# Kernel tuning notes

Measured on AMD Instinct MI355X. Metric: run time of the kernel, lower is better.

## Reference

```python
import jax, jax.numpy as jnp
import numpy as np

B, L, G, HID, H, D = 2, 4096, 256, 768, 12, 64
R = 127            # local_radius
BLK = R + 1        # block_len = 128
N = L // BLK       # 32 blocks (L divisible by BLK)
W = 2 * R + 1      # 255 local window
V = 32             # relative vocab size


def setup_inputs() -> dict:
    ks = jax.random.split(jax.random.key(0), 40)
    inp = {}
    inp["long_input"] = jax.random.normal(ks[0], (B, L, HID), jnp.float32)
    inp["global_input"] = jax.random.normal(ks[1], (B, G, HID), jnp.float32)
    inp["l2l_att_mask"] = jax.random.randint(ks[2], (B, L, W), 0, 2, jnp.int32)
    inp["g2g_att_mask"] = jax.random.randint(ks[3], (B, G, G), 0, 2, jnp.int32)
    inp["l2g_att_mask"] = jax.random.randint(ks[4], (B, L, G), 0, 2, jnp.int32)
    inp["g2l_att_mask"] = jax.random.randint(ks[5], (B, G, L), 0, 2, jnp.int32)
    inp["l2l_relative_att_ids"] = jax.random.randint(ks[6], (B, L, W), 0, V, jnp.int32)
    inp["g2g_relative_att_ids"] = jax.random.randint(ks[7], (B, G, G), 0, V, jnp.int32)
    inp["l2g_relative_att_ids"] = jax.random.randint(ks[8], (B, L, G), 0, V, jnp.int32)
    inp["g2l_relative_att_ids"] = jax.random.randint(ks[9], (B, G, L), 0, V, jnp.int32)
    i = 10
    for nm in ["q_long", "k_long", "v_long", "q_glob", "k_glob", "v_glob"]:
        inp["w" + nm] = 0.02 * jax.random.normal(ks[i], (HID, H * D), jnp.float32); i += 1
        inp["b" + nm] = jnp.zeros((H * D,), jnp.float32)
    inp["rel_emb_long"] = 0.5 * jax.random.normal(ks[i], (V, H, D), jnp.float32); i += 1
    inp["rel_bias_long"] = jnp.zeros((V, H), jnp.float32)
    inp["rel_emb_glob"] = 0.5 * jax.random.normal(ks[i], (V, H, D), jnp.float32); i += 1
    inp["rel_bias_glob"] = jnp.zeros((V, H), jnp.float32)
    inp["wo_long"] = 0.02 * jax.random.normal(ks[i], (H * D, HID), jnp.float32); i += 1
    inp["bo_long"] = jnp.zeros((HID,), jnp.float32)
    inp["wo_glob"] = 0.02 * jax.random.normal(ks[i], (H * D, HID), jnp.float32); i += 1
    inp["bo_glob"] = jnp.zeros((HID,), jnp.float32)
    return inp


def _expand_local(x):
    """[B, L, W] local-window ids -> blocked [B, N, BLK, 3*BLK] (skew + pad),
    zeroing entries outside the local window or outside the sequence."""
    xb = x.reshape(B, N, BLK, W)
    p = jnp.arange(BLK)[:, None]        # query pos within block
    c = jnp.arange(3 * BLK)[None, :]    # key pos within 3-block window
    r = c - p - 1                       # index into the 2R+1 window
    valid = (r >= 0) & (r < W)
    rc = jnp.clip(r, 0, W - 1)
    out = jnp.take_along_axis(xb, jnp.broadcast_to(rc, (B, N, BLK, 3 * BLK)), axis=-1)
    j = (jnp.arange(N)[:, None, None] - 1) * BLK + c  # absolute key position
    valid_full = valid[None] & (j >= 0) & (j < L)     # [N, BLK, 3*BLK]
    return out * valid_full[None].astype(x.dtype)


def reference(long_input, global_input,
              l2l_att_mask, g2g_att_mask, l2g_att_mask, g2l_att_mask,
              l2l_relative_att_ids, g2g_relative_att_ids,
              l2g_relative_att_ids, g2l_relative_att_ids,
              wq_long, bq_long, wk_long, bk_long, wv_long, bv_long,
              wq_glob, bq_glob, wk_glob, bk_glob, wv_glob, bv_glob,
              rel_emb_long, rel_bias_long, rel_emb_glob, rel_bias_glob,
              wo_long, bo_long, wo_glob, bo_glob):
    scale = 1.0 / jnp.sqrt(jnp.float32(D))

    def proj(x, w, b):
        return (x @ w + b).reshape(x.shape[0], x.shape[1], H, D)

    lq, lk, lv = proj(long_input, wq_long, bq_long), proj(long_input, wk_long, bk_long), proj(long_input, wv_long, bv_long)
    gq, gk, gv = proj(global_input, wq_glob, bq_glob), proj(global_input, wk_glob, bk_glob), proj(global_input, wv_glob, bv_glob)

    # ---- long tokens: blocked local attention fused with side (global) keys ----
    qb = lq.reshape(B, N, BLK, H, D)

    def concat3(x):
        xb = x.reshape(B, N, BLK, H, D)
        pad = jnp.zeros_like(xb[:, :1])
        xp = jnp.concatenate([pad, xb, pad], axis=1)  # [B, N+2, BLK, H, D]
        return jnp.concatenate([xp[:, :-2], xp[:, 1:-1], xp[:, 2:]], axis=2)  # [B,N,3BLK,H,D]

    keys = jnp.concatenate([concat3(lk), jnp.broadcast_to(gk[:, None], (B, N, G, H, D))], axis=2)
    vals = jnp.concatenate([concat3(lv), jnp.broadcast_to(gv[:, None], (B, N, G, H, D))], axis=2)

    mask = jnp.concatenate([_expand_local(l2l_att_mask), l2g_att_mask.reshape(B, N, BLK, G)], axis=-1)
    ids = jnp.concatenate([_expand_local(l2l_relative_att_ids), l2g_relative_att_ids.reshape(B, N, BLK, G)], axis=-1)

    scores = jnp.einsum('bnqhd,bnkhd->bnqkh', qb, keys)
    rel_all = jnp.einsum('bnqhd,rhd->bnqrh', qb, rel_emb_long) + rel_bias_long
    rel = jnp.take_along_axis(rel_all, jnp.broadcast_to(ids[..., None], ids.shape + (H,)), axis=3)
    scores = (scores + rel) * scale
    scores = scores - 10000.0 * (1.0 - mask[..., None].astype(scores.dtype))
    probs = jax.nn.softmax(scores, axis=3)
    long_ctx = jnp.einsum('bnqkh,bnkhd->bnqhd', probs, vals).reshape(B, L, H * D)
    long_out = long_ctx @ wo_long + bo_long

    # ---- global tokens: full attention over [global; long] keys ----
    kf = jnp.concatenate([gk, lk], axis=1)
    vf = jnp.concatenate([gv, lv], axis=1)
    gmask = jnp.concatenate([g2g_att_mask, g2l_att_mask], axis=-1)
    gids = jnp.concatenate([g2g_relative_att_ids, g2l_relative_att_ids], axis=-1)
    gs = jnp.einsum('bqhd,bkhd->bqkh', gq, kf)
    grel_all = jnp.einsum('bqhd,rhd->bqrh', gq, rel_emb_glob) + rel_bias_glob
    grel = jnp.take_along_axis(grel_all, jnp.broadcast_to(gids[..., None], gids.shape + (H,)), axis=2)
    gs = (gs + grel) * scale
    gs = gs - 10000.0 * (1.0 - gmask[..., None].astype(gs.dtype))
    gp = jax.nn.softmax(gs, axis=2)
    glob_ctx = jnp.einsum('bqkh,bkhd->bqhd', gp, vf).reshape(B, G, H * D)
    glob_out = glob_ctx @ wo_glob + bo_glob

    return long_out, glob_out
```

## Files before the change

kernel.cpp:

```cpp
#include <hip/hip_runtime.h>
#include <hip/hip_bf16.h>

typedef unsigned short u16;
typedef unsigned char u8;
typedef unsigned int u32;
typedef __attribute__((ext_vector_type(8))) short bf16x8;
typedef __attribute__((ext_vector_type(4))) float f32x4;

#define BB 2
#define LL 4096
#define GG 256
#define HH 12
#define DD 64
#define NB 32
#define WW 255
#define VV 32
#define NCHUNK 17
#define LKEY 640
#define GKEY 4352
#define WMAT 589824

__device__ __forceinline__ float bf2f(u16 u) {
  return __uint_as_float(((unsigned)u) << 16);
}
__device__ __forceinline__ u16 f2bf(float f) {
  unsigned u = __float_as_uint(f);
  u += 0x7FFFu + ((u >> 16) & 1u);
  return (u16)(u >> 16);
}
__device__ __forceinline__ float4 ld4bf(const u16* p) {
  ushort4 q = *reinterpret_cast<const ushort4*>(p);
  return make_float4(bf2f(q.x), bf2f(q.y), bf2f(q.z), bf2f(q.w));
}
__device__ __forceinline__ float ldx1(const void* p, size_t idx, bool f32m) {
  if (f32m) return reinterpret_cast<const float*>(p)[idx];
  return bf2f(reinterpret_cast<const u16*>(p)[idx]);
}
__device__ __forceinline__ void gload16(const u16* src, u16* ldsdst) {
  __builtin_amdgcn_global_load_lds(
      (const __attribute__((address_space(1))) unsigned int*)src,
      (__attribute__((address_space(3))) unsigned int*)ldsdst, 16, 0, 0);
}

__global__ void detect_dtype(const void* __restrict__ x, int* __restrict__ flag) {
  __shared__ int cnt;
  if (threadIdx.x == 0) cnt = 0;
  __syncthreads();
  const u16* p = reinterpret_cast<const u16*>(x);
  int c = 0;
  for (int i = threadIdx.x; i < 4096; i += 256) {
    int e = (p[i] >> 7) & 0xFF;
    if (e >= 134) c++;
  }
  atomicAdd(&cnt, c);
  __syncthreads();
  if (threadIdx.x == 0) *flag = (cnt >= 64) ? 1 : 0;
}

__global__ __launch_bounds__(256)
void pack_l(const int* __restrict__ m_l2l, const int* __restrict__ m_l2g,
            const int* __restrict__ i_l2l, const int* __restrict__ i_l2g,
            u8* __restrict__ pk) {
  const unsigned idx = blockIdx.x * 256u + threadIdx.x;
  const int pos = idx & 63;
  const int lnp = pos >> 2, ktp = pos & 3;
  const int qrow = (idx >> 6) & 127;
  const unsigned rest = idx >> 13;
  const int tile = rest % 10;
  const unsigned bn = rest / 10;
  const int n = bn & 31, b = bn >> 5;
  const int c = (tile << 6) + (ktp << 4) + lnp;
  const unsigned bt = (unsigned)b * LL + (n << 7) + qrow;
  int mask = 0, id = 0;
  if (c < 384) {
    const int rr = c - qrow - 1;
    const int jabs = ((n - 1) << 7) + c;
    if (rr >= 0 && rr < WW && jabs >= 0 && jabs < LL) {
      const size_t base = (size_t)bt * WW + rr;
      mask = m_l2l[base]; id = i_l2l[base];
    }
  } else {
    const size_t base = (size_t)bt * GG + (c - 384);
    mask = m_l2g[base]; id = i_l2g[base];
  }
  pk[idx] = (u8)((id & 31) | ((mask ^ 1) << 7));
}

__global__ __launch_bounds__(256)
void pack_g(const int* __restrict__ m_g2g, const int* __restrict__ m_g2l,
            const int* __restrict__ i_g2g, const int* __restrict__ i_g2l,
            u8* __restrict__ pk) {
  const unsigned idx = blockIdx.x * 256u + threadIdx.x;
  const unsigned c = idx % (unsigned)GKEY;
  const unsigned bq = idx / (unsigned)GKEY;
  int mask, id;
  if (c < 256u) {
    const size_t base = (size_t)bq * GG + c;
    mask = m_g2g[base]; id = i_g2g[base];
  } else {
    const size_t base = (size_t)bq * (size_t)LL + (c - 256u);
    mask = m_g2l[base]; id = i_g2l[base];
  }
  pk[idx] = (u8)((id & 31) | ((mask ^ 1) << 7));
}

__global__ __launch_bounds__(256)
void wprep(const void* __restrict__ W0, const void* __restrict__ W1,
           const void* __restrict__ W2, const void* __restrict__ W3,
           const void* __restrict__ W4, const void* __restrict__ W5,
           u16* __restrict__ wt, const int* __restrict__ flagp) {
  const bool f32m = (*flagp != 0);
  const int mat = blockIdx.z;
  const void* Wm = (mat == 0) ? W0 : (mat == 1) ? W1 : (mat == 2) ? W2
                   : (mat == 3) ? W3 : (mat == 4) ? W4 : W5;
  const int n0 = blockIdx.x << 6, k0 = blockIdx.y << 6;
  const int tid = threadIdx.x;
  __shared__ u16 T[64][72];
  {
    const int r = tid >> 2, c0 = (tid & 3) << 4;
    if (f32m) {
      const float* wp = reinterpret_cast<const float*>(Wm) + (size_t)(k0 + r) * 768 + n0 + c0;
      #pragma unroll
      for (int j = 0; j < 16; j += 4) {
        float4 v = *reinterpret_cast<const float4*>(wp + j);
        T[r][c0 + j + 0] = f2bf(v.x); T[r][c0 + j + 1] = f2bf(v.y);
        T[r][c0 + j + 2] = f2bf(v.z); T[r][c0 + j + 3] = f2bf(v.w);
      }
    } else {
      const u16* wp = reinterpret_cast<const u16*>(Wm) + (size_t)(k0 + r) * 768 + n0 + c0;
      *reinterpret_cast<int4*>(&T[r][c0]) = reinterpret_cast<const int4*>(wp)[0];
      *reinterpret_cast<int4*>(&T[r][c0 + 8]) = reinterpret_cast<const int4*>(wp)[1];
    }
  }
  __syncthreads();
  {
    const int n = tid >> 2, kc0 = (tid & 3) << 4;
    u16 buf[16];
    #pragma unroll
    for (int j = 0; j < 16; j++) buf[j] = T[kc0 + j][n];
    u16* op = wt + ((size_t)mat * WMAT) + (size_t)(n0 + n) * 768 + k0 + kc0;
    *reinterpret_cast<int4*>(op) = *reinterpret_cast<int4*>(buf);
    *reinterpret_cast<int4*>(op + 8) = *reinterpret_cast<int4*>(buf + 8);
  }
}

__global__ __launch_bounds__(256)
void xprep(const void* __restrict__ x, u16* __restrict__ out,
           const int* __restrict__ flagp) {
  const bool f32m = (*flagp != 0);
  const size_t i = ((size_t)blockIdx.x * 256 + threadIdx.x) << 3;
  if (f32m) {
    const float* p = reinterpret_cast<const float*>(x) + i;
    float4 a = *reinterpret_cast<const float4*>(p);
    float4 b = *reinterpret_cast<const float4*>(p + 4);
    u16 o[8] = {f2bf(a.x), f2bf(a.y), f2bf(a.z), f2bf(a.w),
                f2bf(b.x), f2bf(b.y), f2bf(b.z), f2bf(b.w)};
    *reinterpret_cast<int4*>(out + i) = *reinterpret_cast<int4*>(o);
  } else {
    *reinterpret_cast<int4*>(out + i) =
        *reinterpret_cast<const int4*>(reinterpret_cast<const u16*>(x) + i);
  }
}

#define GEMM_CORE(A_, Wt_, row0_, ncol0_)                                        \
  __shared__ u16 lds[16384];                                                     \
  const int tid = threadIdx.x;                                                   \
  const int w = tid >> 6, l = tid & 63;                                          \
  const int lm = l & 15, quad = l >> 4;                                          \
  const int wr = w >> 1, wc = w & 1;                                             \
  const int rb = (w << 5) + (l >> 3);                                            \
  const int c8 = (l & 7) ^ (l >> 3);                                             \
  const u16* asrc = A_ + (size_t)(row0_ + rb) * 768 + (c8 << 3);                 \
  const u16* bsrc = Wt_ + (size_t)(ncol0_ + rb) * 768 + (c8 << 3);               \
  u16* adst = lds + (w << 11) + (l << 3);                                        \
  u16* bdst = adst + 8192;                                                       \
  f32x4 acc[4][4];                                                               \
  _Pragma("unroll")                                                              \
  for (int mt = 0; mt < 4; mt++)                                                 \
    _Pragma("unroll")                                                            \
    for (int nt = 0; nt < 4; nt++) acc[mt][nt] = (f32x4){0.f, 0.f, 0.f, 0.f};    \
  const char* abase = reinterpret_cast<const char*>(lds);                        \
  const char* bbase = abase + 16384;                                             \
  const int xorv = (lm & 7) << 4;                                                \
  for (int k0 = 0; k0 < 768; k0 += 64) {                                         \
    __syncthreads();                                                             \
    _Pragma("unroll")                                                            \
    for (int i = 0; i < 4; i++) gload16(asrc + k0 + i * 6144, adst + (i << 9));  \
    _Pragma("unroll")                                                            \
    for (int i = 0; i < 4; i++) gload16(bsrc + k0 + i * 6144, bdst + (i << 9));  \
    __syncthreads();                                                             \
    _Pragma("unroll")                                                            \
    for (int kk = 0; kk < 2; kk++) {                                             \
      bf16x8 af[4], bfr[4];                                                      \
      _Pragma("unroll")                                                          \
      for (int mt = 0; mt < 4; mt++)                                             \
        af[mt] = *reinterpret_cast<const bf16x8*>(                               \
            abase + ((wr << 6) + (mt << 4) + lm) * 128 +                         \
            (((kk << 6) + (quad << 4)) ^ xorv));                                 \
      _Pragma("unroll")                                                          \
      for (int nt = 0; nt < 4; nt++)                                             \
        bfr[nt] = *reinterpret_cast<const bf16x8*>(                              \
            bbase + ((wc << 6) + (nt << 4) + lm) * 128 +                         \
            (((kk << 6) + (quad << 4)) ^ xorv));                                 \
      _Pragma("unroll")                                                          \
      for (int mt = 0; mt < 4; mt++)                                             \
        _Pragma("unroll")                                                        \
        for (int nt = 0; nt < 4; nt++)                                           \
          acc[mt][nt] = __builtin_amdgcn_mfma_f32_16x16x32_bf16(                 \
              af[mt], bfr[nt], acc[mt][nt], 0, 0, 0);                            \
    }                                                                            \
  }

__global__ __launch_bounds__(256)
void gemm_qkv(const u16* __restrict__ A, const u16* __restrict__ Wt,
              const void* __restrict__ b0, const void* __restrict__ b1,
              const void* __restrict__ b2,
              u16* __restrict__ C0, u16* __restrict__ C1, u16* __restrict__ C2,
              const int* __restrict__ flagp) {
  const bool f32m = (*flagp != 0);
  int lx = blockIdx.x, ly = blockIdx.y;
  if (gridDim.y == 64) {
    const int fid = blockIdx.x + gridDim.x * blockIdx.y;
    const int x = fid & 7, r = fid >> 3;
    ly = (x << 3) | (r & 7);
    lx = r >> 3;
  }
  const int row0 = ly << 7;
  const int ncol0 = lx << 7;
  GEMM_CORE(A, Wt, row0, ncol0)

  const int which = lx / 6;
  const void* bias = (which == 0) ? b0 : ((which == 1) ? b1 : b2);
  u16* Cv = (which == 0) ? C0 : ((which == 1) ? C1 : C2);
  const float sc = (which == 0) ? 0.125f : 1.0f;
  const int colw = (lx % 6) << 7;
  #pragma unroll
  for (int nt = 0; nt < 4; nt++) {
    const int gcol = colw + (wc << 6) + (nt << 4) + lm;
    const float bv = ldx1(bias, gcol, f32m);
    #pragma unroll
    for (int mt = 0; mt < 4; mt++)
      #pragma unroll
      for (int r = 0; r < 4; r++) {
        const int grow = row0 + (wr << 6) + (mt << 4) + (quad << 2) + r;
        Cv[(size_t)grow * 768 + gcol] = f2bf((acc[mt][nt][r] + bv) * sc);
      }
  }
}

__global__ __launch_bounds__(256)
void gemm_out(const u16* __restrict__ A, const u16* __restrict__ Wt,
              const void* __restrict__ bias, void* __restrict__ Cv,
              size_t c_off, const int* __restrict__ flagp) {
  const bool f32m = (*flagp != 0);
  int lx = blockIdx.x, ly = blockIdx.y;
  if (gridDim.y == 64) {
    const int fid = blockIdx.x + gridDim.x * blockIdx.y;
    const int x = fid & 7, r = fid >> 3;
    ly = (x << 3) | (r & 7);
    lx = r >> 3;
  }
  const int row0 = ly << 7;
  const int ncol0 = lx << 7;
  GEMM_CORE(A, Wt, row0, ncol0)

  #pragma unroll
  for (int nt = 0; nt < 4; nt++) {
    const int gcol = ncol0 + (wc << 6) + (nt << 4) + lm;
    const float bv = ldx1(bias, gcol, f32m);
    #pragma unroll
    for (int mt = 0; mt < 4; mt++)
      #pragma unroll
      for (int r = 0; r < 4; r++) {
        const int grow = row0 + (wr << 6) + (mt << 4) + (quad << 2) + r;
        const float v = acc[mt][nt][r] + bv;
        if (f32m)
          reinterpret_cast<float*>(Cv)[c_off + (size_t)grow * 768 + gcol] = v;
        else
          reinterpret_cast<u16*>(Cv)[c_off + (size_t)grow * 768 + gcol] = f2bf(v);
      }
  }
}

__global__ __launch_bounds__(256)
void relk(const u16* __restrict__ Q, const void* __restrict__ emb,
          const void* __restrict__ bias, u16* __restrict__ outp, int T,
          const int* __restrict__ flagp) {
  const bool f32m = (*flagp != 0);
  const int h = blockIdx.y, b = blockIdx.z;
  const int t0 = blockIdx.x << 6;
  const int tid = threadIdx.x;
  __shared__ float Qst[64][68];
  __shared__ float Es[64][36];
  #pragma unroll
  for (int i = 0; i < 4; i++) {
    const int idx = tid + (i << 8);
    const int tt = idx >> 4, d = (idx & 15) << 2;
    float4 v = ld4bf(Q + (((size_t)b * T + t0 + tt) * HH + h) * DD + d);
    Qst[d + 0][tt] = v.x; Qst[d + 1][tt] = v.y;
    Qst[d + 2][tt] = v.z; Qst[d + 3][tt] = v.w;
  }
  #pragma unroll
  for (int i = 0; i < 8; i++) {
    const int idx = tid + (i << 8);
    const int r = idx >> 6, d = idx & 63;
    Es[d][r] = ldx1(emb, ((size_t)r * HH + h) * DD + d, f32m);
  }
  __syncthreads();
  const int tq = (tid & 31) << 1;
  const int r0 = (tid >> 5) << 2;
  float acc[2][4] = {};
  #pragma unroll 8
  for (int d = 0; d < 64; d++) {
    float2 qq = *reinterpret_cast<const float2*>(&Qst[d][tq]);
    float4 e = *reinterpret_cast<const float4*>(&Es[d][r0]);
    acc[0][0] += qq.x * e.x; acc[0][1] += qq.x * e.y;
    acc[0][2] += qq.x * e.z; acc[0][3] += qq.x * e.w;
    acc[1][0] += qq.y * e.x; acc[1][1] += qq.y * e.y;
    acc[1][2] += qq.y * e.z; acc[1][3] += qq.y * e.w;
  }
  float bv[4];
  #pragma unroll
  for (int j = 0; j < 4; j++) bv[j] = ldx1(bias, (size_t)(r0 + j) * HH + h, f32m) * 0.125f;
  #pragma unroll
  for (int i = 0; i < 2; i++) {
    ushort4 o;
    o.x = f2bf(acc[i][0] + bv[0]); o.y = f2bf(acc[i][1] + bv[1]);
    o.z = f2bf(acc[i][2] + bv[2]); o.w = f2bf(acc[i][3] + bv[3]);
    *reinterpret_cast<ushort4*>(&outp[(((size_t)b * T + t0 + tq + i) * HH + h) * VV + r0]) = o;
  }
}

__global__ __launch_bounds__(512)
void lattn(const u16* __restrict__ lq, const u16* __restrict__ lk, const u16* __restrict__ lv,
           const u16* __restrict__ gk, const u16* __restrict__ gv,
           const u32* __restrict__ pkl, const u16* __restrict__ rel,
           u16* __restrict__ lctx) {
  const int fid = blockIdx.x + 12 * (blockIdx.y + (blockIdx.z << 5));
  const int hg = fid >> 3;
  const int h = hg % 12;
  const int fl = (fid & 7) + ((hg / 12) << 3);
  const int n = fl & 31, b = fl >> 5;
  const int tid = threadIdx.x;
  __shared__ u16 Kt[64][72];
  __shared__ u16 Vt[64][74];
  __shared__ u16 Pt[128][76];
  __shared__ u16 Rl[128][36];

  const int lane = tid & 63, wv = tid >> 6;
  const int ln = lane & 15, quad = lane >> 4;
  const int tbase = n << 7;

  {
    const int qr = (wv << 4) + (lane >> 2);
    const int seg = (lane & 3) << 3;
    *reinterpret_cast<int4*>(&Rl[qr][seg]) = *reinterpret_cast<const int4*>(
        rel + (((size_t)b * LL + tbase + qr) * HH + h) * VV + seg);
  }

  bf16x8 aq[2];
  {
    const int t = tbase + (wv << 4) + ln;
    const u16* qp = lq + (((size_t)b * LL + t) * HH + h) * DD + (quad << 3);
    aq[0] = *reinterpret_cast<const bf16x8*>(qp);
    aq[1] = *reinterpret_cast<const bf16x8*>(qp + 32);
  }

  const u32* pk32 = pkl + (size_t)(b * 32 + n) * 20480;
  const int skey = tid >> 3, sdg = (tid & 7) << 3;
  const int scol = ((skey & 15) << 2) | (skey >> 4);

  f32x4 Oacc[4];
  #pragma unroll
  for (int dt = 0; dt < 4; dt++) Oacc[dt] = (f32x4){0.f, 0.f, 0.f, 0.f};
  float lpart[4] = {};

  for (int tile = 0; tile < 10; tile++) {
    const int c0 = tile << 6;
    const bool isg = (tile >= 6);

    float badd[16];
    #pragma unroll
    for (int r = 0; r < 4; r++) {
      const int qrow = (wv << 4) + (quad << 2) + r;
      const u32 pw = pk32[(((tile << 7) + qrow) << 4) + ln];
      #pragma unroll
      for (int kt = 0; kt < 4; kt++) {
        const u32 pb = (pw >> (kt << 3)) & 0xFFu;
        const float rv = bf2f(Rl[qrow][pb & 31]);
        badd[(kt << 2) + r] = (pb & 0x80u) ? (rv - 10000.f) : rv;
      }
    }

    __syncthreads();
    {
      int4 kraw = {0, 0, 0, 0}, vraw = {0, 0, 0, 0};
      if (isg) {
        const size_t base = (((size_t)b * GG + (c0 - 384) + skey) * HH + h) * DD + sdg;
        kraw = *reinterpret_cast<const int4*>(gk + base);
        vraw = *reinterpret_cast<const int4*>(gv + base);
      } else {
        const int jabs = ((n - 1) << 7) + c0 + skey;
        if (jabs >= 0 && jabs < LL) {
          const size_t base = (((size_t)b * LL + jabs) * HH + h) * DD + sdg;
          kraw = *reinterpret_cast<const int4*>(lk + base);
          vraw = *reinterpret_cast<const int4*>(lv + base);
        }
      }
      *reinterpret_cast<int4*>(&Kt[skey][sdg]) = kraw;
      u16 vb[8];
      *reinterpret_cast<int4*>(vb) = vraw;
      #pragma unroll
      for (int j = 0; j < 8; j++) Vt[sdg + j][scol] = vb[j];
    }
    __syncthreads();

    f32x4 Sacc[4];
    #pragma unroll
    for (int kt = 0; kt < 4; kt++) Sacc[kt] = (f32x4){0.f, 0.f, 0.f, 0.f};
    __builtin_amdgcn_s_setprio(1);
    #pragma unroll
    for (int kk = 0; kk < 2; kk++) {
      bf16x8 bk[4];
      #pragma unroll
      for (int kt = 0; kt < 4; kt++)
        bk[kt] = *reinterpret_cast<const bf16x8*>(&Kt[(kt << 4) + ln][(kk << 5) + (quad << 3)]);
      #pragma unroll
      for (int kt = 0; kt < 4; kt++)
        Sacc[kt] = __builtin_amdgcn_mfma_f32_16x16x32_bf16(aq[kk], bk[kt], Sacc[kt], 0, 0, 0);
    }
    __builtin_amdgcn_s_setprio(0);

    #pragma unroll
    for (int r = 0; r < 4; r++) {
      const int ql = (wv << 4) + (quad << 2) + r;
      const float p0 = __expf(Sacc[0][r] + badd[0 + r]);
      const float p1 = __expf(Sacc[1][r] + badd[4 + r]);
      const float p2 = __expf(Sacc[2][r] + badd[8 + r]);
      const float p3 = __expf(Sacc[3][r] + badd[12 + r]);
      u32 w0, w1;
      asm("v_cvt_pk_bf16_f32 %0, %1, %2" : "=v"(w0) : "v"(p0), "v"(p1));
      asm("v_cvt_pk_bf16_f32 %0, %1, %2" : "=v"(w1) : "v"(p2), "v"(p3));
      uint2 wp; wp.x = w0; wp.y = w1;
      *reinterpret_cast<uint2*>(&Pt[ql][ln << 2]) = wp;
      lpart[r] += __uint_as_float(w0 << 16) + __uint_as_float(w0 & 0xFFFF0000u)
                + __uint_as_float(w1 << 16) + __uint_as_float(w1 & 0xFFFF0000u);
    }

    __builtin_amdgcn_s_setprio(1);
    #pragma unroll
    for (int kk = 0; kk < 2; kk++) {
      bf16x8 ap = *reinterpret_cast<const bf16x8*>(&Pt[(wv << 4) + ln][(kk << 5) + (quad << 3)]);
      #pragma unroll
      for (int dt = 0; dt < 4; dt++) {
        bf16x8 bv = *reinterpret_cast<const bf16x8*>(&Vt[(dt << 4) + ln][(kk << 5) + (quad << 3)]);
        Oacc[dt] = __builtin_amdgcn_mfma_f32_16x16x32_bf16(ap, bv, Oacc[dt], 0, 0, 0);
      }
    }
    __builtin_amdgcn_s_setprio(0);
  }

  #pragma unroll
  for (int r = 0; r < 4; r++) {
    float v = lpart[r];
    v += __shfl_xor(v, 1); v += __shfl_xor(v, 2);
    v += __shfl_xor(v, 4); v += __shfl_xor(v, 8);
    const float inv = 1.0f / v;
    const int t = tbase + (wv << 4) + (quad << 2) + r;
    const size_t base = (((size_t)b * LL + t) * HH + h) * DD;
    #pragma unroll
    for (int dt = 0; dt < 4; dt++)
      lctx[base + (dt << 4) + ln] = f2bf(Oacc[dt][r] * inv);
  }
}

__global__ __launch_bounds__(256)
void gattn(const u16* __restrict__ gq, const u16* __restrict__ gk, const u16* __restrict__ gv,
           const u16* __restrict__ lk, const u16* __restrict__ lv,
           const u8* __restrict__ pkg, const u16* __restrict__ relg,
           float* __restrict__ po, float* __restrict__ pl) {
  const int fid = blockIdx.x + 12 * (blockIdx.y + 17 * blockIdx.z);
  const int hg = fid >> 3;
  const int h = hg % 12;
  const int fl = (fid & 7) + ((hg / 12) << 3);
  const int chunk = fl % 17;
  const int bqt = fl / 17;
  const int b = bqt >> 2, qt = bqt & 3;
  const int tid = threadIdx.x;
  __shared__ u16 Kt[64][72];
  __shared__ u16 Vt[64][74];
  __shared__ u16 Pt[64][74];
  __shared__ u16 Rg[64][36];

  const int lane = tid & 63, wv = tid >> 6;
  const int ln = lane & 15, quad = lane >> 4;
  const int kbase = chunk << 8;
  const bool isgg = (chunk == 0);

  {
    const int qr = (wv << 4) + (lane >> 2);
    const int seg = (lane & 3) << 3;
    *reinterpret_cast<int4*>(&Rg[qr][seg]) = *reinterpret_cast<const int4*>(
        relg + (((size_t)b * GG + (qt << 6) + qr) * HH + h) * VV + seg);
  }

  bf16x8 aq[2];
  {
    const int qa = (qt << 6) + (wv << 4) + ln;
    const u16* qp = gq + (((size_t)b * GG + qa) * HH + h) * DD + (quad << 3);
    aq[0] = *reinterpret_cast<const bf16x8*>(qp);
    aq[1] = *reinterpret_cast<const bf16x8*>(qp + 32);
  }

  const u8* pkb = pkg + ((size_t)b * GG + (qt << 6)) * GKEY;

  f32x4 Oacc[4];
  #pragma unroll
  for (int dt = 0; dt < 4; dt++) Oacc[dt] = (f32x4){0.f, 0.f, 0.f, 0.f};
  float lpart[4] = {};

  for (int tile = 0; tile < 4; tile++) {
    const int c0 = kbase + (tile << 6);

    float badd[16];
    #pragma unroll
    for (int r = 0; r < 4; r++) {
      const int qrow = (wv << 4) + (quad << 2) + r;
      const u8* prow = pkb + qrow * GKEY + c0 + ln;
      #pragma unroll
      for (int kt = 0; kt < 4; kt++) {
        const u8 pb = prow[kt << 4];
        const float rv = bf2f(Rg[qrow][pb & 31]);
        badd[(kt << 2) + r] = (pb & 0x80) ? (rv - 10000.f) : rv;
      }
    }

    __syncthreads();
    #pragma unroll
    for (int p = 0; p < 2; p++) {
      const int idx = tid + (p << 8);
      const int key = idx >> 3, dg = (idx & 7) << 3;
      const int kc = c0 + key;
      int4 kraw, vraw;
      if (isgg) {
        const size_t base = (((size_t)b * GG + kc) * HH + h) * DD + dg;
        kraw = *reinterpret_cast<const int4*>(gk + base);
        vraw = *reinterpret_cast<const int4*>(gv + base);
      } else {
        const size_t base = (((size_t)b * LL + (kc - 256)) * HH + h) * DD + dg;
        kraw = *reinterpret_cast<const int4*>(lk + base);
        vraw = *reinterpret_cast<const int4*>(lv + base);
      }
      *reinterpret_cast<int4*>(&Kt[key][dg]) = kraw;
      u16 vb[8];
      *reinterpret_cast<int4*>(vb) = vraw;
      #pragma unroll
      for (int j = 0; j < 8; j++) Vt[dg + j][key] = vb[j];
    }
    __syncthreads();

    f32x4 Sacc[4];
    #pragma unroll
    for (int kt = 0; kt < 4; kt++) Sacc[kt] = (f32x4){0.f, 0.f, 0.f, 0.f};
    __builtin_amdgcn_s_setprio(1);
    #pragma unroll
    for (int kk = 0; kk < 2; kk++) {
      bf16x8 bk[4];
      #pragma unroll
      for (int kt = 0; kt < 4; kt++)
        bk[kt] = *reinterpret_cast<const bf16x8*>(&Kt[(kt << 4) + ln][(kk << 5) + (quad << 3)]);
      #pragma unroll
      for (int kt = 0; kt < 4; kt++)
        Sacc[kt] = __builtin_amdgcn_mfma_f32_16x16x32_bf16(aq[kk], bk[kt], Sacc[kt], 0, 0, 0);
    }
    __builtin_amdgcn_s_setprio(0);

    #pragma unroll
    for (int kt = 0; kt < 4; kt++)
      #pragma unroll
      for (int r = 0; r < 4; r++) {
        const int ql = (wv << 4) + (quad << 2) + r;
        const float s = Sacc[kt][r] + badd[(kt << 2) + r];
        const u16 p16 = f2bf(__expf(s));
        Pt[ql][(kt << 4) + ln] = p16;
        lpart[r] += bf2f(p16);
      }

    __builtin_amdgcn_s_setprio(1);
    #pragma unroll
    for (int kk = 0; kk < 2; kk++) {
      bf16x8 ap = *reinterpret_cast<const bf16x8*>(&Pt[(wv << 4) + ln][(kk << 5) + (quad << 3)]);
      #pragma unroll
      for (int dt = 0; dt < 4; dt++) {
        bf16x8 bv = *reinterpret_cast<const bf16x8*>(&Vt[(dt << 4) + ln][(kk << 5) + (quad << 3)]);
        Oacc[dt] = __builtin_amdgcn_mfma_f32_16x16x32_bf16(ap, bv, Oacc[dt], 0, 0, 0);
      }
    }
    __builtin_amdgcn_s_setprio(0);
  }

  #pragma unroll
  for (int r = 0; r < 4; r++) {
    float v = lpart[r];
    v += __shfl_xor(v, 1); v += __shfl_xor(v, 2);
    v += __shfl_xor(v, 4); v += __shfl_xor(v, 8);
    const int qa = (qt << 6) + (wv << 4) + (quad << 2) + r;
    if (ln == 0)
      pl[(((size_t)chunk * BB + b) * HH + h) * GG + qa] = v;
    const size_t base = ((((size_t)chunk * BB + b) * HH + h) * GG + qa) * DD;
    #pragma unroll
    for (int dt = 0; dt < 4; dt++)
      po[base + (dt << 4) + ln] = Oacc[dt][r];
  }
}

__global__ __launch_bounds__(256)
void gcombine(const float* __restrict__ po, const float* __restrict__ pl,
              u16* __restrict__ gctx) {
  const int flat = blockIdx.x * 256 + threadIdx.x;
  const int d = flat & 63;
  const int rest = flat >> 6;
  const int h = rest % HH;
  const int bq = rest / HH;
  const int b = bq >> 8, qg = bq & 255;
  float so = 0.f, sl = 0.f;
  #pragma unroll
  for (int c = 0; c < NCHUNK; c++) {
    so += po[((((size_t)c * BB + b) * HH + h) * GG + qg) * DD + d];
    sl += pl[(((size_t)c * BB + b) * HH + h) * GG + qg];
  }
  gctx[flat] = f2bf(so / sl);
}

extern "C" void kernel_launch(void* const* d_in, const int* in_sizes, int n_in,
                              void* d_out, int out_size, void* d_ws, size_t ws_size,
                              hipStream_t stream) {
  (void)in_sizes; (void)n_in; (void)out_size; (void)ws_size;
  const void* x_long = d_in[0];
  const void* x_glob = d_in[1];
  const int* m_l2l = (const int*)d_in[2];
  const int* m_g2g = (const int*)d_in[3];
  const int* m_l2g = (const int*)d_in[4];
  const int* m_g2l = (const int*)d_in[5];
  const int* i_l2l = (const int*)d_in[6];
  const int* i_g2g = (const int*)d_in[7];
  const int* i_l2g = (const int*)d_in[8];
  const int* i_g2l = (const int*)d_in[9];
  const void* wq_l = d_in[10]; const void* bq_l = d_in[11];
  const void* wk_l = d_in[12]; const void* bk_l = d_in[13];
  const void* wv_l = d_in[14]; const void* bv_l = d_in[15];
  const void* wq_g = d_in[16]; const void* bq_g = d_in[17];
  const void* wk_g = d_in[18]; const void* bk_g = d_in[19];
  const void* wv_g = d_in[20]; const void* bv_g = d_in[21];
  const void* rel_emb_l = d_in[22]; const void* rel_bias_l = d_in[23];
  const void* rel_emb_g = d_in[24]; const void* rel_bias_g = d_in[25];
  const void* wo_l = d_in[26]; const void* bo_l = d_in[27];
  const void* wo_g = d_in[28]; const void* bo_g = d_in[29];

  constexpr size_t NLQ = (size_t)BB * LL * HH * DD;
  constexpr size_t NG  = (size_t)BB * GG * HH * DD;
  constexpr size_t NRL = (size_t)BB * LL * HH * VV;
  constexpr size_t NRG = (size_t)BB * GG * HH * VV;
  u16* lqw  = reinterpret_cast<u16*>(d_ws);
  u16* lkw  = lqw + NLQ;
  u16* lvw  = lkw + NLQ;
  u16* gqw  = lvw + NLQ;
  u16* gkw  = gqw + NG;
  u16* gvw  = gkw + NG;
  u16* rell = gvw + NG;
  u16* relg = rell + NRL;
  u16* lctx = relg + NRG;
  u16* gctx = lctx + NLQ;
  int* flag = reinterpret_cast<int*>(gctx + NG);
  float* po = reinterpret_cast<float*>(flag + 16);
  float* pl = po + (size_t)NCHUNK * BB * HH * GG * DD;
  u8* pk_l = reinterpret_cast<u8*>(po);
  u16* wt_qkv = reinterpret_cast<u16*>(po) + 2621440;
  u16* xl_bf = lctx;
  u16* xg_bf = gctx;
  u8* pk_g = reinterpret_cast<u8*>(pl + (size_t)NCHUNK * BB * HH * GG);
  u16* wt_o = reinterpret_cast<u16*>(pk_g + (size_t)BB * GG * GKEY);

  dim3 t256(256);
  detect_dtype<<<1, t256, 0, stream>>>(x_long, flag);
  pack_l<<<dim3((BB * LL * LKEY) / 256), t256, 0, stream>>>(m_l2l, m_l2g, i_l2l, i_l2g, pk_l);
  pack_g<<<dim3((BB * GG * GKEY) / 256), t256, 0, stream>>>(m_g2g, m_g2l, i_g2g, i_g2l, pk_g);
  wprep<<<dim3(12, 12, 6), t256, 0, stream>>>(wq_l, wk_l, wv_l, wq_g, wk_g, wv_g, wt_qkv, flag);
  wprep<<<dim3(12, 12, 2), t256, 0, stream>>>(wo_l, wo_g, wo_l, wo_l, wo_l, wo_l, wt_o, flag);
  xprep<<<dim3((BB * LL * 768) / 2048), t256, 0, stream>>>(x_long, xl_bf, flag);
  xprep<<<dim3((BB * GG * 768) / 2048), t256, 0, stream>>>(x_glob, xg_bf, flag);
  gemm_qkv<<<dim3(18, 64), t256, 0, stream>>>(xl_bf, wt_qkv, bq_l, bk_l, bv_l,
                                              lqw, lkw, lvw, flag);
  gemm_qkv<<<dim3(18, 4), t256, 0, stream>>>(xg_bf, wt_qkv + (size_t)3 * WMAT,
                                             bq_g, bk_g, bv_g, gqw, gkw, gvw, flag);
  relk<<<dim3(64, 12, 2), t256, 0, stream>>>(lqw, rel_emb_l, rel_bias_l, rell, LL, flag);
  relk<<<dim3(4, 12, 2), t256, 0, stream>>>(gqw, rel_emb_g, rel_bias_g, relg, GG, flag);
  lattn<<<dim3(12, 32, 2), dim3(512), 0, stream>>>(lqw, lkw, lvw, gkw, gvw,
                                                   reinterpret_cast<const u32*>(pk_l), rell, lctx);
  gattn<<<dim3(12, NCHUNK, 8), t256, 0, stream>>>(gqw, gkw, gvw, lkw, lvw,
                                                  pk_g, relg, po, pl);
  gcombine<<<dim3(1536), t256, 0, stream>>>(po, pl, gctx);
  gemm_out<<<dim3(6, 64), t256, 0, stream>>>(lctx, wt_o, bo_l, d_out, 0, flag);
  gemm_out<<<dim3(6, 4), t256, 0, stream>>>(gctx, wt_o + WMAT, bo_g, d_out,
                                            (size_t)BB * LL * 768, flag);
}
```

Baseline: 428.8 us.

## Widen gattn to 128-query blocks with pre-swizzled packed mask layout

```diff
diff --git a/kernel.cpp b/kernel.cpp
--- a/kernel.cpp
+++ b/kernel.cpp
@@ -91,14 +91,21 @@
             const int* __restrict__ i_g2g, const int* __restrict__ i_g2l,
             u8* __restrict__ pk) {
   const unsigned idx = blockIdx.x * 256u + threadIdx.x;
-  const unsigned c = idx % (unsigned)GKEY;
-  const unsigned bq = idx / (unsigned)GKEY;
+  const int pos = idx & 63;
+  const int lnp = pos >> 2, ktp = pos & 3;
+  const int qrow = (idx >> 6) & 127;
+  const unsigned rest = idx >> 13;
+  const int tl = rest % 68;
+  const unsigned b2q = rest / 68;
+  const int b = b2q >> 1, qtp = b2q & 1;
+  const int c = (tl << 6) + (ktp << 4) + lnp;
+  const int q = (qtp << 7) + qrow;
   int mask, id;
-  if (c < 256u) {
-    const size_t base = (size_t)bq * GG + c;
+  if (c < 256) {
+    const size_t base = ((size_t)b * GG + q) * GG + c;
     mask = m_g2g[base]; id = i_g2g[base];
   } else {
-    const size_t base = (size_t)bq * (size_t)LL + (c - 256u);
+    const size_t base = ((size_t)b * GG + q) * (size_t)LL + (c - 256);
     mask = m_g2l[base]; id = i_g2l[base];
   }
   pk[idx] = (u8)((id & 31) | ((mask ^ 1) << 7));
@@ -443,8 +450,7 @@
       asm("v_cvt_pk_bf16_f32 %0, %1, %2" : "=v"(w1) : "v"(p2), "v"(p3));
       uint2 wp; wp.x = w0; wp.y = w1;
       *reinterpret_cast<uint2*>(&Pt[ql][ln << 2]) = wp;
-      lpart[r] += __uint_as_float(w0 << 16) + __uint_as_float(w0 & 0xFFFF0000u)
-                + __uint_as_float(w1 << 16) + __uint_as_float(w1 & 0xFFFF0000u);
+      lpart[r] += (p0 + p1) + (p2 + p3);
     }
 
     __builtin_amdgcn_s_setprio(1);
@@ -474,26 +480,29 @@
   }
 }
 
-__global__ __launch_bounds__(256)
+__global__ __launch_bounds__(512)
 void gattn(const u16* __restrict__ gq, const u16* __restrict__ gk, const u16* __restrict__ gv,
            const u16* __restrict__ lk, const u16* __restrict__ lv,
-           const u8* __restrict__ pkg, const u16* __restrict__ relg,
+           const u32* __restrict__ pkg, const u16* __restrict__ relg,
            float* __restrict__ po, float* __restrict__ pl) {
-  const int fid = blockIdx.x + 12 * (blockIdx.y + 17 * blockIdx.z);
-  const int hg = fid >> 3;
-  const int h = hg % 12;
-  const int fl = (fid & 7) + ((hg / 12) << 3);
-  const int chunk = fl % 17;
-  const int bqt = fl / 17;
-  const int b = bqt >> 2, qt = bqt & 3;
+  const int fid = blockIdx.x;
+  const int x = fid & 7;
+  const int slot = fid >> 3;
+  const int qtp = slot & 1;
+  const int g = ((slot >> 1) << 3) | x;
+  const int h = g % 12;
+  const int cb = g / 12;
+  const int chunk = cb % 17;
+  const int b = cb / 17;
   const int tid = threadIdx.x;
   __shared__ u16 Kt[64][72];
   __shared__ u16 Vt[64][74];
-  __shared__ u16 Pt[64][74];
-  __shared__ u16 Rg[64][36];
+  __shared__ u16 Pt[128][76];
+  __shared__ u16 Rg[128][36];
 
   const int lane = tid & 63, wv = tid >> 6;
   const int ln = lane & 15, quad = lane >> 4;
+  const int qbase = qtp << 7;
   const int kbase = chunk << 8;
   const bool isgg = (chunk == 0);
 
@@ -501,18 +510,20 @@
     const int qr = (wv << 4) + (lane >> 2);
     const int seg = (lane & 3) << 3;
     *reinterpret_cast<int4*>(&Rg[qr][seg]) = *reinterpret_cast<const int4*>(
-        relg + (((size_t)b * GG + (qt << 6) + qr) * HH + h) * VV + seg);
+        relg + (((size_t)b * GG + qbase + qr) * HH + h) * VV + seg);
   }
 
   bf16x8 aq[2];
   {
-    const int qa = (qt << 6) + (wv << 4) + ln;
+    const int qa = qbase + (wv << 4) + ln;
     const u16* qp = gq + (((size_t)b * GG + qa) * HH + h) * DD + (quad << 3);
     aq[0] = *reinterpret_cast<const bf16x8*>(qp);
     aq[1] = *reinterpret_cast<const bf16x8*>(qp + 32);
   }
 
-  const u8* pkb = pkg + ((size_t)b * GG + (qt << 6)) * GKEY;
+  const u32* pk32 = pkg + (size_t)((b << 1) + qtp) * 139264;
+  const int skey = tid >> 3, sdg = (tid & 7) << 3;
+  const int scol = ((skey & 15) << 2) | (skey >> 4);
 
   f32x4 Oacc[4];
   #pragma unroll
@@ -520,42 +531,39 @@
   float lpart[4] = {};
 
   for (int tile = 0; tile < 4; tile++) {
-    const int c0 = kbase + (tile << 6);
+    const int tl = (chunk << 2) + tile;
 
     float badd[16];
     #pragma unroll
     for (int r = 0; r < 4; r++) {
       const int qrow = (wv << 4) + (quad << 2) + r;
-      const u8* prow = pkb + qrow * GKEY + c0 + ln;
+      const u32 pw = pk32[(((tl << 7) + qrow) << 4) + ln];
       #pragma unroll
       for (int kt = 0; kt < 4; kt++) {
-        const u8 pb = prow[kt << 4];
+        const u32 pb = (pw >> (kt << 3)) & 0xFFu;
         const float rv = bf2f(Rg[qrow][pb & 31]);
-        badd[(kt << 2) + r] = (pb & 0x80) ? (rv - 10000.f) : rv;
+        badd[(kt << 2) + r] = (pb & 0x80u) ? (rv - 10000.f) : rv;
       }
     }
 
     __syncthreads();
-    #pragma unroll
-    for (int p = 0; p < 2; p++) {
-      const int idx = tid + (p << 8);
-      const int key = idx >> 3, dg = (idx & 7) << 3;
-      const int kc = c0 + key;
+    {
+      const int kc = kbase + (tile << 6) + skey;
       int4 kraw, vraw;
       if (isgg) {
-        const size_t base = (((size_t)b * GG + kc) * HH + h) * DD + dg;
+        const size_t base = (((size_t)b * GG + kc) * HH + h) * DD + sdg;
         kraw = *reinterpret_cast<const int4*>(gk + base);
         vraw = *reinterpret_cast<const int4*>(gv + base);
       } else {
-        const size_t base = (((size_t)b * LL + (kc - 256)) * HH + h) * DD + dg;
+        const size_t base = (((size_t)b * LL + (kc - 256)) * HH + h) * DD + sdg;
         kraw = *reinterpret_cast<const int4*>(lk + base);
         vraw = *reinterpret_cast<const int4*>(lv + base);
       }
-      *reinterpret_cast<int4*>(&Kt[key][dg]) = kraw;
+      *reinterpret_cast<int4*>(&Kt[skey][sdg]) = kraw;
       u16 vb[8];
       *reinterpret_cast<int4*>(vb) = vraw;
       #pragma unroll
-      for (int j = 0; j < 8; j++) Vt[dg + j][key] = vb[j];
+      for (int j = 0; j < 8; j++) Vt[sdg + j][scol] = vb[j];
     }
     __syncthreads();
 
@@ -576,15 +584,19 @@
     __builtin_amdgcn_s_setprio(0);
 
     #pragma unroll
-    for (int kt = 0; kt < 4; kt++)
-      #pragma unroll
-      for (int r = 0; r < 4; r++) {
-        const int ql = (wv << 4) + (quad << 2) + r;
-        const float s = Sacc[kt][r] + badd[(kt << 2) + r];
-        const u16 p16 = f2bf(__expf(s));
-        Pt[ql][(kt << 4) + ln] = p16;
-        lpart[r] += bf2f(p16);
-      }
+    for (int r = 0; r < 4; r++) {
+      const int ql = (wv << 4) + (quad << 2) + r;
+      const float p0 = __expf(Sacc[0][r] + badd[0 + r]);
+      const float p1 = __expf(Sacc[1][r] + badd[4 + r]);
+      const float p2 = __expf(Sacc[2][r] + badd[8 + r]);
+      const float p3 = __expf(Sacc[3][r] + badd[12 + r]);
+      u32 w0, w1;
+      asm("v_cvt_pk_bf16_f32 %0, %1, %2" : "=v"(w0) : "v"(p0), "v"(p1));
+      asm("v_cvt_pk_bf16_f32 %0, %1, %2" : "=v"(w1) : "v"(p2), "v"(p3));
+      uint2 wp; wp.x = w0; wp.y = w1;
+      *reinterpret_cast<uint2*>(&Pt[ql][ln << 2]) = wp;
+      lpart[r] += (p0 + p1) + (p2 + p3);
+    }
 
     __builtin_amdgcn_s_setprio(1);
     #pragma unroll
@@ -604,7 +616,7 @@
     float v = lpart[r];
     v += __shfl_xor(v, 1); v += __shfl_xor(v, 2);
     v += __shfl_xor(v, 4); v += __shfl_xor(v, 8);
-    const int qa = (qt << 6) + (wv << 4) + (quad << 2) + r;
+    const int qa = qbase + (wv << 4) + (quad << 2) + r;
     if (ln == 0)
       pl[(((size_t)chunk * BB + b) * HH + h) * GG + qa] = v;
     const size_t base = ((((size_t)chunk * BB + b) * HH + h) * GG + qa) * DD;
@@ -697,8 +709,8 @@
   relk<<<dim3(4, 12, 2), t256, 0, stream>>>(gqw, rel_emb_g, rel_bias_g, relg, GG, flag);
   lattn<<<dim3(12, 32, 2), dim3(512), 0, stream>>>(lqw, lkw, lvw, gkw, gvw,
                                                    reinterpret_cast<const u32*>(pk_l), rell, lctx);
-  gattn<<<dim3(12, NCHUNK, 8), t256, 0, stream>>>(gqw, gkw, gvw, lkw, lvw,
-                                                  pk_g, relg, po, pl);
+  gattn<<<dim3(816), dim3(512), 0, stream>>>(gqw, gkw, gvw, lkw, lvw,
+                                             reinterpret_cast<const u32*>(pk_g), relg, po, pl);
   gcombine<<<dim3(1536), t256, 0, stream>>>(po, pl, gctx);
   gemm_out<<<dim3(6, 64), t256, 0, stream>>>(lctx, wt_o, bo_l, d_out, 0, flag);
   gemm_out<<<dim3(6, 4), t256, 0, stream>>>(gctx, wt_o + WMAT, bo_g, d_out,
```

After: 418.9 us. -2.3%, faster.
